# Kernel tuning notes

Hardware: AMD Instinct MI355X
Metric: run time of the kernel (lower is better)

Reference implementation:

```python
import jax, jax.numpy as jnp
import numpy as np

N, M, FEAT, POS, D, MSG, NCLS = 64, 32, 256, 6, 262, 128, 7


def setup_inputs() -> dict:
    key = jax.random.key(0)
    ks = jax.random.split(key, 12)
    s = 0.05
    p = lambda k, shape: jax.random.normal(k, shape, jnp.float32) * s
    return {
        "nodes_feature": jax.random.normal(ks[0], (N, M, FEAT), jnp.float32),
        "pos": jax.random.normal(ks[1], (N, M, POS), jnp.float32),
        "num_rec": jax.random.randint(ks[2], (N,), 1, M + 1),
        "link_w1": p(ks[3], (D, 2 * D)),
        "link_b1": jnp.zeros((D,), jnp.float32),
        "link_w2": p(ks[4], (D,)),
        "link_b2": jnp.zeros((), jnp.float32),
        "msg_w": p(ks[5], (MSG, D)),
        "msg_b": jnp.zeros((MSG,), jnp.float32),
        "gru_w_ih": p(ks[6], (3 * D, MSG)),
        "gru_w_hh": p(ks[7], (3 * D, D)),
        "gru_b_ih": jnp.zeros((3 * D,), jnp.float32),
        "gru_b_hh": jnp.zeros((3 * D,), jnp.float32),
        "ro_w1": p(ks[8], (MSG, D)),
        "ro_b1": jnp.zeros((MSG,), jnp.float32),
        "ro_w2": p(ks[9], (NCLS, MSG)),
        "ro_b2": jnp.zeros((NCLS,), jnp.float32),
    }


def reference(nodes_feature, pos, num_rec, link_w1, link_b1, link_w2, link_b2,
              msg_w, msg_b, gru_w_ih, gru_w_hh, gru_b_ih, gru_b_hh,
              ro_w1, ro_b1, ro_w2, ro_b2):
    # node_feat = [resnet_feat, pos]  -> (N, M, 262)
    nf = jnp.concatenate([nodes_feature, pos], axis=-1)
    n, m, d = nf.shape
    valid = jnp.arange(m)[None, :] < num_rec[:, None]          # (N, M)
    pair = valid[:, :, None] & valid[:, None, :]               # (N, M, M)

    # edge_feat[b,:,i,j] = concat(nf[b,i], nf[b,j]); zero for invalid pairs
    ef = jnp.concatenate([
        jnp.broadcast_to(nf[:, :, None, :], (n, m, m, d)),
        jnp.broadcast_to(nf[:, None, :, :], (n, m, m, d)),
    ], axis=-1) * pair[..., None].astype(nf.dtype)             # (N, M, M, 2D)

    # 1x1 convs == per-pair MLP
    hlink = jax.nn.relu(jnp.einsum('bnwc,dc->bnwd', ef, link_w1) + link_b1)
    attmat = jax.nn.sigmoid(jnp.einsum('bnwd,d->bnw', hlink, link_w2) + link_b2)

    # messages are only summed over valid sender nodes w
    att_m = attmat * valid[:, None, :].astype(attmat.dtype)    # (N, M, M)

    def gru_step(x, h):
        # PyTorch GRU cell: gates order (r, z, n)
        gx = x @ gru_w_ih.T + gru_b_ih
        gh = h @ gru_w_hh.T + gru_b_hh
        xr, xz, xn = jnp.split(gx, 3, axis=-1)
        hr, hz, hn = jnp.split(gh, 3, axis=-1)
        r = jax.nn.sigmoid(xr + hr)
        z = jax.nn.sigmoid(xz + hz)
        c = jnp.tanh(xn + r * hn)
        return (1.0 - z) * c + z * h

    vmask = valid[..., None].astype(nf.dtype)
    h_state = nf                                               # pass 0 input state
    for _ in range(2):                                         # two message-passing rounds
        msg = h_state @ msg_w.T + msg_b                        # (N, M, 128)
        m_v = jnp.einsum('bnw,bwk->bnk', att_m, msg)           # attention-weighted sum
        h_state = gru_step(m_v, h_state) * vmask               # invalid nodes stay zero

    pred = (jax.nn.relu(h_state @ ro_w1.T + ro_b1) @ ro_w2.T + ro_b2) * vmask
    return pred, attmat
```

## Files before the change

kernel.cpp:

```cpp
#include <hip/hip_runtime.h>
#include <math.h>

#define N_G   64
#define M_N   32
#define FEAT  256
#define POSD  6
#define D     262
#define MSG   128
#define NCLS  7

#define KA_S  424
#define PSTR  320

#define O_WPROJ 0u
#define O_WMSG  76032u
#define O_WRZ   94464u
#define O_WXN   207616u
#define O_WHN   225024u
#define O_WRO   264192u
#define O_WRO2  282624u
#define O_GB    283648u

typedef __attribute__((ext_vector_type(8))) short short8;
typedef __attribute__((ext_vector_type(4))) short short4v;
typedef __attribute__((ext_vector_type(4))) float floatx4;

#define MFMA __builtin_amdgcn_mfma_f32_16x16x32_bf16

__device__ __forceinline__ short f2bf(float f) {
    union { float f; unsigned u; } v; v.f = f;
    unsigned r = v.u + 0x7FFF + ((v.u >> 16) & 1);
    return (short)(r >> 16);
}
__device__ __forceinline__ float bf2f(short s) {
    union { float f; unsigned u; } v;
    v.u = ((unsigned)(unsigned short)s) << 16;
    return v.f;
}
__device__ __forceinline__ float sigf(float x) {
    return __builtin_amdgcn_rcpf(1.f + __expf(-x));
}
__device__ __forceinline__ float tanh_fast(float x) {
    float e = __expf(-2.f * fabsf(x));
    float t = (1.f - e) * __builtin_amdgcn_rcpf(1.f + e);
    return copysignf(t, x);
}

__global__ __launch_bounds__(256) void prep_kernel(
    const float* __restrict__ w1, const float* __restrict__ msg_w,
    const float* __restrict__ w_ih, const float* __restrict__ w_hh,
    const float* __restrict__ ro_w1, const float* __restrict__ ro_w2,
    const float* __restrict__ b_ih, const float* __restrict__ b_hh,
    float* __restrict__ ws)
{
    short* wproj = (short*)(ws + O_WPROJ);
    short* wmsg  = (short*)(ws + O_WMSG);
    short* wrz   = (short*)(ws + O_WRZ);
    short* wxn   = (short*)(ws + O_WXN);
    short* whn   = (short*)(ws + O_WHN);
    short* wro   = (short*)(ws + O_WRO);
    short* wro2  = (short*)(ws + O_WRO2);
    float* gb    = ws + O_GB;

    int job = blockIdx.x * 4 + (threadIdx.x >> 6);
    const int lane = threadIdx.x & 63;
    if (job >= 1112) return;
    const int lrow = lane & 15, quad = lane >> 4;

    if (job < 297) {
        const int s = job / 9, kk = job % 9;
        const int n = s * 16 + lrow, kb = quad * 8 + kk * 32;
        short8 o;
#pragma unroll
        for (int e = 0; e < 8; ++e) {
            int k = kb + e;
            float v = 0.f;
            if (k < D && n < 524)
                v = (n < D) ? w1[n * 524 + k] : w1[(n - D) * 524 + D + k];
            o[e] = f2bf(v);
        }
        *(short8*)(wproj + job * 512 + lane * 8) = o;
        return;
    }
    job -= 297;
    if (job < 72) {
        const int s = job / 9, kk = job % 9;
        const int n = s * 16 + lrow, kb = quad * 8 + kk * 32;
        short8 o;
#pragma unroll
        for (int e = 0; e < 8; ++e) {
            int k = kb + e;
            o[e] = f2bf(k < D ? msg_w[n * D + k] : 0.f);
        }
        *(short8*)(wmsg + job * 512 + lane * 8) = o;
        return;
    }
    job -= 72;
    if (job < 442) {
        const int gi = job >= 221;
        const int jj = job - gi * 221;
        const int s = jj / 13, kk = jj % 13;
        const int d = s * 16 + lrow, kb = quad * 8 + kk * 32;
        short8 o;
#pragma unroll
        for (int e = 0; e < 8; ++e) {
            int k = kb + e;
            float v = 0.f;
            if (d < D) {
                int r = gi * D + d;
                if (k < 128)          v = w_ih[r * MSG + k];
                else if (k < 128 + D) v = w_hh[r * D + (k - 128)];
            }
            o[e] = f2bf(v);
        }
        *(short8*)(wrz + job * 512 + lane * 8) = o;
        return;
    }
    job -= 442;
    if (job < 68) {
        const int s = job / 4, kk = job % 4;
        const int d = s * 16 + lrow, kb = quad * 8 + kk * 32;
        short8 o;
#pragma unroll
        for (int e = 0; e < 8; ++e) {
            int k = kb + e;
            o[e] = f2bf(d < D ? w_ih[(2 * D + d) * MSG + k] : 0.f);
        }
        *(short8*)(wxn + job * 512 + lane * 8) = o;
        return;
    }
    job -= 68;
    if (job < 153) {
        const int s = job / 9, kk = job % 9;
        const int d = s * 16 + lrow, kb = quad * 8 + kk * 32;
        short8 o;
#pragma unroll
        for (int e = 0; e < 8; ++e) {
            int k = kb + e;
            o[e] = f2bf((d < D && k < D) ? w_hh[(2 * D + d) * D + k] : 0.f);
        }
        *(short8*)(whn + job * 512 + lane * 8) = o;
        return;
    }
    job -= 153;
    if (job < 72) {
        const int s = job / 9, kk = job % 9;
        const int n = s * 16 + lrow, kb = quad * 8 + kk * 32;
        short8 o;
#pragma unroll
        for (int e = 0; e < 8; ++e) {
            int k = kb + e;
            o[e] = f2bf(k < D ? ro_w1[n * D + k] : 0.f);
        }
        *(short8*)(wro + job * 512 + lane * 8) = o;
        return;
    }
    job -= 72;
    if (job < 4) {
        const int kk = job;
        const int n = lrow, kb = quad * 8 + kk * 32;
        short8 o;
#pragma unroll
        for (int e = 0; e < 8; ++e) {
            int k = kb + e;
            o[e] = f2bf(n < NCLS ? ro_w2[n * MSG + k] : 0.f);
        }
        *(short8*)(wro2 + job * 512 + lane * 8) = o;
        return;
    }
    job -= 4;
    {
        const int seg = job;
        float* out = gb + seg * 272;
        for (int d = lane; d < 272; d += 64) {
            float v = 0.f;
            if (d < D) {
                if (seg == 0)      v = b_ih[d] + b_hh[d];
                else if (seg == 1) v = b_ih[D + d] + b_hh[D + d];
                else if (seg == 2) v = b_ih[2 * D + d];
                else               v = b_hh[2 * D + d];
            }
            out[d] = v;
        }
    }
}

__global__ __launch_bounds__(512, 2) void fused_kernel(
    const float* __restrict__ nodes, const float* __restrict__ pos,
    const int* __restrict__ nrec_g,
    const float* __restrict__ b1g, const float* __restrict__ w2g,
    const float* __restrict__ b2g, const float* __restrict__ msg_bg,
    const float* __restrict__ ro_b1g, const float* __restrict__ ro_b2g,
    const float* __restrict__ ws,
    float* __restrict__ att_out, float* __restrict__ pred)
{
    const short* Wproj = (const short*)(ws + O_WPROJ);
    const short* Wmsg  = (const short*)(ws + O_WMSG);
    const short* Wrz   = (const short*)(ws + O_WRZ);
    const short* Wxn   = (const short*)(ws + O_WXN);
    const short* Whn   = (const short*)(ws + O_WHN);
    const short* Wro   = (const short*)(ws + O_WRO);
    const short* Wro2  = (const short*)(ws + O_WRO2);
    const float* gb    = ws + O_GB;

    __shared__ __align__(16) short bufA[32 * KA_S];
    __shared__ __align__(16) short bufB[32 * KA_S];
    __shared__ __align__(16) short paL[32 * PSTR];
    __shared__ __align__(16) short pbL[32 * PSTR];
    __shared__ __align__(16) short attL[32 * 40];
    __shared__ __align__(16) short msgT[128 * 40];
    __shared__ __align__(16) short hidL[32 * 136];
    __shared__ __align__(16) float b1L[PSTR], w2L[PSTR];

    const int b = blockIdx.x;
    const int tid = threadIdx.x;
    const int wave = tid >> 6, lane = tid & 63;
    const int quad = lane >> 4, lrow = lane & 15;

    floatx4 prm[10];
    {
        const floatx4* pb = (const floatx4*)(ws + O_WRZ);
        const int base = wave * 64 + lane;
#pragma unroll
        for (int p = 0; p < 10; ++p)
            prm[p] = pb[(p * 512 + base) * 8];
    }
    short8 wvA[9];
    {
        const short* bw = Wproj + wave * 9 * 512 + lane * 8;
#pragma unroll
        for (int kk = 0; kk < 9; ++kk) wvA[kk] = *(const short8*)(bw + kk * 512);
    }

    const int nr = nrec_g[b];

    for (int idx = tid; idx < 32 * 64; idx += 512) {
        int w = idx >> 6, c4 = idx & 63;
        floatx4 v = *(const floatx4*)(nodes + ((size_t)(b * 32 + w)) * FEAT + c4 * 4);
        short4v s; s[0] = f2bf(v[0]); s[1] = f2bf(v[1]); s[2] = f2bf(v[2]); s[3] = f2bf(v[3]);
        *(short4v*)(bufA + w * KA_S + 128 + c4 * 4) = s;
    }
    for (int idx = tid; idx < 32 * POSD; idx += 512) {
        int w = idx / POSD, c = idx % POSD;
        bufA[w * KA_S + 128 + FEAT + c] = f2bf(pos[((size_t)(b * 32 + w)) * POSD + c]);
    }
    for (int idx = tid; idx < 32 * 34; idx += 512) {
        int w = idx / 34, c = idx % 34;
        bufA[w * KA_S + 390 + c] = 0;
        bufB[w * KA_S + 390 + c] = 0;
    }
    for (int idx = tid; idx < 32 * (PSTR - D); idx += 512) {
        int w = idx / (PSTR - D), c = idx % (PSTR - D);
        paL[w * PSTR + D + c] = 0;
        pbL[w * PSTR + D + c] = 0;
    }
    for (int d = tid; d < PSTR; d += 512) {
        b1L[d] = (d < D) ? b1g[d] : 0.f;
        w2L[d] = (d < D) ? w2g[d] : 0.f;
    }
#pragma unroll
    for (int p = 0; p < 10; ++p) asm volatile("" :: "v"(prm[p]));
    __syncthreads();

    {
        auto store_proj = [&](int s, floatx4 acc0, floatx4 acc1) {
            int col = s * 16 + lrow;
#pragma unroll
            for (int rr = 0; rr < 4; ++rr) {
                int r0 = quad * 4 + rr;
                if (col < D) {
                    paL[r0 * PSTR + col] = f2bf(acc0[rr]);
                    paL[(r0 + 16) * PSTR + col] = f2bf(acc1[rr]);
                } else if (col < 2 * D) {
                    pbL[r0 * PSTR + (col - D)] = f2bf(acc0[rr]);
                    pbL[(r0 + 16) * PSTR + (col - D)] = f2bf(acc1[rr]);
                }
            }
        };
        auto store_msg = [&](int s, floatx4 acc0, floatx4 acc1) {
            int col = (s - 33) * 16 + lrow;
            float bias = msg_bg[col];
#pragma unroll
            for (int rr = 0; rr < 4; ++rr) {
                msgT[col * 40 + quad * 4 + rr] = f2bf(acc0[rr] + bias);
                msgT[col * 40 + 16 + quad * 4 + rr] = f2bf(acc1[rr] + bias);
            }
        };

        short8 aF0[9], aF1[9];
        {
            const short* ap = bufA + lrow * KA_S + 128 + quad * 8;
#pragma unroll
            for (int kk = 0; kk < 9; ++kk) {
                aF0[kk] = *(const short8*)(ap + kk * 32);
                aF1[kk] = *(const short8*)(ap + 16 * KA_S + kk * 32);
            }
#pragma unroll
            for (int kk = 0; kk < 9; ++kk)
                asm volatile("" : "+v"(aF0[kk]), "+v"(aF1[kk]));
        }
        short8 wvB[9];

#define P1_LOAD(DST, TT) do { \
            const short* bw_ = ((TT) < 33) \
                ? Wproj + (TT) * 9 * 512 + lane * 8 \
                : Wmsg + ((TT) - 33) * 9 * 512 + lane * 8; \
            _Pragma("unroll") \
            for (int kk = 0; kk < 9; ++kk) DST[kk] = *(const short8*)(bw_ + kk * 512); \
        } while (0)

#define P1_TILE(W, TT) do { \
            floatx4 acc0_ = {}, acc1_ = {}; \
            _Pragma("unroll") \
            for (int kk = 0; kk < 9; ++kk) { \
                acc0_ = MFMA(aF0[kk], W[kk], acc0_, 0, 0, 0); \
                acc1_ = MFMA(aF1[kk], W[kk], acc1_, 0, 0, 0); \
            } \
            if ((TT) < 33) store_proj((TT), acc0_, acc1_); \
            else store_msg((TT), acc0_, acc1_); \
        } while (0)

        int t = wave;
        P1_LOAD(wvB, t + 8);
        P1_TILE(wvA, t);
        t += 8;
        P1_LOAD(wvA, t + 8);
        P1_TILE(wvB, t);
        t += 8;
        P1_LOAD(wvB, t + 8);
        P1_TILE(wvA, t);
        t += 8;
        P1_LOAD(wvA, t + 8);
        P1_TILE(wvB, t);
        t += 8;
        if (t + 8 < 41) P1_LOAD(wvB, t + 8);
        P1_TILE(wvA, t);
        t += 8;
        if (t < 41) P1_TILE(wvB, t);
#undef P1_LOAD
#undef P1_TILE
    }
    __syncthreads();

    {
        const int grp = tid >> 4;
        const int c16 = tid & 15;
        const float b2v = b2g[0];
        float pav[5][4], b1v[5][4], w2v[5][4];
#pragma unroll
        for (int k = 0; k < 5; ++k) {
            int dbase = c16 * 4 + 64 * k;
            short4v p = *(const short4v*)(paL + grp * PSTR + dbase);
            floatx4 bb = *(const floatx4*)(b1L + dbase);
            floatx4 ww = *(const floatx4*)(w2L + dbase);
#pragma unroll
            for (int e = 0; e < 4; ++e) {
                pav[k][e] = bf2f(p[e]); b1v[k][e] = bb[e]; w2v[k][e] = ww[e];
            }
        }
        float p0 = 0.f;
#pragma unroll
        for (int k = 0; k < 5; ++k)
#pragma unroll
            for (int e = 0; e < 4; ++e)
                p0 += fmaxf(b1v[k][e], 0.f) * w2v[k][e];
        p0 += __shfl_down(p0, 8, 16); p0 += __shfl_down(p0, 4, 16);
        p0 += __shfl_down(p0, 2, 16); p0 += __shfl_down(p0, 1, 16);
        float c0 = sigf(p0 + b2v);
        const bool vi = grp < nr;
        for (int j = 0; j < 32; ++j) {
            float a;
            if (j < nr && vi) {
                const short* pb = pbL + j * PSTR + c16 * 4;
                float s = 0.f;
#pragma unroll
                for (int k = 0; k < 5; ++k) {
                    short4v q = *(const short4v*)(pb + 64 * k);
#pragma unroll
                    for (int e = 0; e < 4; ++e) {
                        float v = pav[k][e] + bf2f(q[e]) + b1v[k][e];
                        s += fmaxf(v, 0.f) * w2v[k][e];
                    }
                }
                s += __shfl_down(s, 8, 16); s += __shfl_down(s, 4, 16);
                s += __shfl_down(s, 2, 16); s += __shfl_down(s, 1, 16);
                a = sigf(s + b2v);
            } else {
                a = c0;
            }
            if (c16 == 0) {
                att_out[((size_t)(b * 32 + grp)) * 32 + j] = a;
                attL[grp * 40 + j] = f2bf((j < nr) ? a : 0.f);
            }
        }
    }
    __syncthreads();

    for (int rnd = 0; rnd < 2; ++rnd) {
        short* src = rnd ? bufB : bufA;
        short* dst = rnd ? bufA : bufB;

        if (rnd) {
            int s = wave;
            const short* bw = Wmsg + s * 9 * 512 + lane * 8;
            short8 wm[9];
#pragma unroll
            for (int kk = 0; kk < 9; ++kk) wm[kk] = *(const short8*)(bw + kk * 512);
            floatx4 acc0 = {}, acc1 = {};
            const short* ap = src + lrow * KA_S + 128 + quad * 8;
#pragma unroll
            for (int kk = 0; kk < 9; ++kk) {
                short8 x0 = *(const short8*)(ap + kk * 32);
                short8 x1 = *(const short8*)(ap + 16 * KA_S + kk * 32);
                acc0 = MFMA(x0, wm[kk], acc0, 0, 0, 0);
                acc1 = MFMA(x1, wm[kk], acc1, 0, 0, 0);
            }
            int col = s * 16 + lrow;
            float bias = msg_bg[col];
#pragma unroll
            for (int rr = 0; rr < 4; ++rr) {
                msgT[col * 40 + quad * 4 + rr] = f2bf(acc0[rr] + bias);
                msgT[col * 40 + 16 + quad * 4 + rr] = f2bf(acc1[rr] + bias);
            }
            __syncthreads();
        }

        {
            int mi = wave & 1, ng = wave >> 1;
            short8 afrag = *(const short8*)(attL + (mi * 16 + lrow) * 40 + quad * 8);
            floatx4 acc0 = {}, acc1 = {};
            short8 bf0 = *(const short8*)(msgT + (ng * 32 + lrow) * 40 + quad * 8);
            short8 bf1 = *(const short8*)(msgT + (ng * 32 + 16 + lrow) * 40 + quad * 8);
            acc0 = MFMA(afrag, bf0, acc0, 0, 0, 0);
            acc1 = MFMA(afrag, bf1, acc1, 0, 0, 0);
#pragma unroll
            for (int rr = 0; rr < 4; ++rr) {
                int m = mi * 16 + quad * 4 + rr;
                src[m * KA_S + ng * 32 + lrow] = f2bf(acc0[rr]);
                src[m * KA_S + ng * 32 + 16 + lrow] = f2bf(acc1[rr]);
            }
        }
        __syncthreads();

        {
            short8 aA0[13], aA1[13];
            {
                const short* ap0 = src + lrow * KA_S + quad * 8;
#pragma unroll
                for (int kk = 0; kk < 13; ++kk) {
                    aA0[kk] = *(const short8*)(ap0 + kk * 32);
                    aA1[kk] = *(const short8*)(ap0 + 16 * KA_S + kk * 32);
                }
#pragma unroll
                for (int kk = 0; kk < 13; ++kk)
                    asm volatile("" : "+v"(aA0[kk]), "+v"(aA1[kk]));
            }
            for (int s = wave; s < 17; s += 8) {
                const short* bpr = Wrz + (s * 13) * 512 + lane * 8;
                const short* bpz = Wrz + (221 + s * 13) * 512 + lane * 8;
                const short* bpx = Wxn + (s * 4) * 512 + lane * 8;
                const short* bph = Whn + (s * 9) * 512 + lane * 8;

                short8 wr[13];
#pragma unroll
                for (int kk = 0; kk < 13; ++kk) wr[kk] = *(const short8*)(bpr + kk * 512);
#pragma unroll
                for (int kk = 0; kk < 13; ++kk) asm volatile("" : "+v"(wr[kk]));

                floatx4 aR0 = {}, aR1 = {}, aZ0 = {}, aZ1 = {};
                floatx4 aN0 = {}, aN1 = {}, aH0 = {}, aH1 = {};
#pragma unroll
                for (int kk = 0; kk < 13; ++kk) {
                    aR0 = MFMA(aA0[kk], wr[kk], aR0, 0, 0, 0);
                    aR1 = MFMA(aA1[kk], wr[kk], aR1, 0, 0, 0);
                    if (kk < 4) {
                        short8 bx = *(const short8*)(bpx + kk * 512);
                        aN0 = MFMA(aA0[kk], bx, aN0, 0, 0, 0);
                        aN1 = MFMA(aA1[kk], bx, aN1, 0, 0, 0);
                    }
                    wr[kk] = *(const short8*)(bpz + kk * 512);
                }
#pragma unroll
                for (int kk = 0; kk < 13; ++kk) {
                    aZ0 = MFMA(aA0[kk], wr[kk], aZ0, 0, 0, 0);
                    aZ1 = MFMA(aA1[kk], wr[kk], aZ1, 0, 0, 0);
                    if (kk < 9) wr[kk] = *(const short8*)(bph + kk * 512);
                }
#pragma unroll
                for (int kk = 0; kk < 9; ++kk) {
                    aH0 = MFMA(aA0[kk + 4], wr[kk], aH0, 0, 0, 0);
                    aH1 = MFMA(aA1[kk + 4], wr[kk], aH1, 0, 0, 0);
                }

                int d = s * 16 + lrow;
                if (d < D) {
                    float bgr = gb[d], bgz = gb[272 + d];
                    float bxv = gb[544 + d], bhv = gb[816 + d];
#pragma unroll
                    for (int i = 0; i < 2; ++i) {
                        floatx4 vR = i ? aR1 : aR0, vZ = i ? aZ1 : aZ0;
                        floatx4 vN = i ? aN1 : aN0, vH = i ? aH1 : aH0;
#pragma unroll
                        for (int rr = 0; rr < 4; ++rr) {
                            int m = i * 16 + quad * 4 + rr;
                            float rg = sigf(vR[rr] + bgr);
                            float zg = sigf(vZ[rr] + bgz);
                            float cg = tanh_fast(vN[rr] + bxv + rg * (vH[rr] + bhv));
                            float hold = bf2f(src[m * KA_S + 128 + d]);
                            float hv = (1.f - zg) * cg + zg * hold;
                            if (m >= nr) hv = 0.f;
                            dst[m * KA_S + 128 + d] = f2bf(hv);
                        }
                    }
                }
            }
        }
        __syncthreads();
    }

    {
        int s = wave;
        const short* bw = Wro + s * 9 * 512 + lane * 8;
        short8 wv[9];
#pragma unroll
        for (int kk = 0; kk < 9; ++kk) wv[kk] = *(const short8*)(bw + kk * 512);
        floatx4 acc0 = {}, acc1 = {};
        const short* ap = bufA + lrow * KA_S + 128 + quad * 8;
#pragma unroll
        for (int kk = 0; kk < 9; ++kk) {
            short8 x0 = *(const short8*)(ap + kk * 32);
            short8 x1 = *(const short8*)(ap + 16 * KA_S + kk * 32);
            acc0 = MFMA(x0, wv[kk], acc0, 0, 0, 0);
            acc1 = MFMA(x1, wv[kk], acc1, 0, 0, 0);
        }
        int col = s * 16 + lrow;
        float bias = ro_b1g[col];
#pragma unroll
        for (int rr = 0; rr < 4; ++rr) {
            hidL[(quad * 4 + rr) * 136 + col] = f2bf(fmaxf(acc0[rr] + bias, 0.f));
            hidL[(16 + quad * 4 + rr) * 136 + col] = f2bf(fmaxf(acc1[rr] + bias, 0.f));
        }
    }
    __syncthreads();

    if (wave == 0) {
        const short* bw = Wro2 + lane * 8;
        short8 wv[4];
#pragma unroll
        for (int kk = 0; kk < 4; ++kk) wv[kk] = *(const short8*)(bw + kk * 512);
        floatx4 acc0 = {}, acc1 = {};
        const short* ap = hidL + lrow * 136 + quad * 8;
#pragma unroll
        for (int kk = 0; kk < 4; ++kk) {
            short8 x0 = *(const short8*)(ap + kk * 32);
            short8 x1 = *(const short8*)(ap + 16 * 136 + kk * 32);
            acc0 = MFMA(x0, wv[kk], acc0, 0, 0, 0);
            acc1 = MFMA(x1, wv[kk], acc1, 0, 0, 0);
        }
        int q = lrow;
        if (q < NCLS) {
            float bias = ro_b2g[q];
#pragma unroll
            for (int i = 0; i < 2; ++i) {
#pragma unroll
                for (int rr = 0; rr < 4; ++rr) {
                    int m = i * 16 + quad * 4 + rr;
                    float v = (i ? acc1[rr] : acc0[rr]) + bias;
                    if (m >= nr) v = 0.f;
                    pred[((size_t)(b * 32 + m)) * NCLS + q] = v;
                }
            }
        }
    }
}

extern "C" void kernel_launch(void* const* d_in, const int* in_sizes, int n_in,
                              void* d_out, int out_size, void* d_ws, size_t ws_size,
                              hipStream_t stream)
{
    const float* nodes = (const float*)d_in[0];
    const float* pos   = (const float*)d_in[1];
    const int*   nrec  = (const int*)d_in[2];
    const float* w1    = (const float*)d_in[3];
    const float* b1    = (const float*)d_in[4];
    const float* w2    = (const float*)d_in[5];
    const float* b2    = (const float*)d_in[6];
    const float* msg_w = (const float*)d_in[7];
    const float* msg_b = (const float*)d_in[8];
    const float* w_ih  = (const float*)d_in[9];
    const float* w_hh  = (const float*)d_in[10];
    const float* b_ih  = (const float*)d_in[11];
    const float* b_hh  = (const float*)d_in[12];
    const float* ro_w1 = (const float*)d_in[13];
    const float* ro_b1 = (const float*)d_in[14];
    const float* ro_w2 = (const float*)d_in[15];
    const float* ro_b2 = (const float*)d_in[16];
    float* ws   = (float*)d_ws;
    float* pred = (float*)d_out;
    float* attout = pred + (size_t)N_G * M_N * NCLS;

    prep_kernel<<<278, 256, 0, stream>>>(w1, msg_w, w_ih, w_hh, ro_w1, ro_w2,
                                         b_ih, b_hh, ws);
    fused_kernel<<<N_G, 512, 0, stream>>>(nodes, pos, nrec, b1, w2, b2, msg_b,
                                          ro_b1, ro_b2, ws, attout, pred);
}
```

Before: 137.4 us.

## Double block size to 1024 threads and redistribute work across sixteen waves

Each block now launches 1024 threads instead of 512, and every phase is re-split across 16 waves. The projection tiles, attention rows (each thread group handles half the columns), message and readout MFMAs (one 16-row half per wave) and the GRU gate tiles are all divided more finely. Register-held A fragments and prefetched weights are dropped in favour of per-iteration LDS and global loads, which frees registers for the larger block. The aim is more latency hiding on a grid of only 64 blocks, at the cost of more LDS and global load traffic and a poorly balanced GRU loop with 17 tiles spread over 16 waves.

```diff
diff --git a/kernel.cpp b/kernel.cpp
--- a/kernel.cpp
+++ b/kernel.cpp
@@ -185,7 +185,7 @@
     }
 }
 
-__global__ __launch_bounds__(512, 2) void fused_kernel(
+__global__ __launch_bounds__(1024, 4) void fused_kernel(
     const float* __restrict__ nodes, const float* __restrict__ pos,
     const int* __restrict__ nrec_g,
     const float* __restrict__ b1g, const float* __restrict__ w2g,
@@ -216,14 +216,15 @@
     const int tid = threadIdx.x;
     const int wave = tid >> 6, lane = tid & 63;
     const int quad = lane >> 4, lrow = lane & 15;
-
-    floatx4 prm[10];
+    const int nr = nrec_g[b];
+
+    floatx4 prm[6];
     {
         const floatx4* pb = (const floatx4*)(ws + O_WRZ);
         const int base = wave * 64 + lane;
 #pragma unroll
-        for (int p = 0; p < 10; ++p)
-            prm[p] = pb[(p * 512 + base) * 8];
+        for (int p = 0; p < 6; ++p)
+            prm[p] = pb[(p * 1024 + base) * 8];
     }
     short8 wvA[9];
     {
@@ -232,34 +233,32 @@
         for (int kk = 0; kk < 9; ++kk) wvA[kk] = *(const short8*)(bw + kk * 512);
     }
 
-    const int nr = nrec_g[b];
-
-    for (int idx = tid; idx < 32 * 64; idx += 512) {
+    for (int idx = tid; idx < 32 * 64; idx += 1024) {
         int w = idx >> 6, c4 = idx & 63;
         floatx4 v = *(const floatx4*)(nodes + ((size_t)(b * 32 + w)) * FEAT + c4 * 4);
         short4v s; s[0] = f2bf(v[0]); s[1] = f2bf(v[1]); s[2] = f2bf(v[2]); s[3] = f2bf(v[3]);
         *(short4v*)(bufA + w * KA_S + 128 + c4 * 4) = s;
     }
-    for (int idx = tid; idx < 32 * POSD; idx += 512) {
+    for (int idx = tid; idx < 32 * POSD; idx += 1024) {
         int w = idx / POSD, c = idx % POSD;
         bufA[w * KA_S + 128 + FEAT + c] = f2bf(pos[((size_t)(b * 32 + w)) * POSD + c]);
     }
-    for (int idx = tid; idx < 32 * 34; idx += 512) {
+    for (int idx = tid; idx < 32 * 34; idx += 1024) {
         int w = idx / 34, c = idx % 34;
         bufA[w * KA_S + 390 + c] = 0;
         bufB[w * KA_S + 390 + c] = 0;
     }
-    for (int idx = tid; idx < 32 * (PSTR - D); idx += 512) {
+    for (int idx = tid; idx < 32 * (PSTR - D); idx += 1024) {
         int w = idx / (PSTR - D), c = idx % (PSTR - D);
         paL[w * PSTR + D + c] = 0;
         pbL[w * PSTR + D + c] = 0;
     }
-    for (int d = tid; d < PSTR; d += 512) {
+    for (int d = tid; d < PSTR; d += 1024) {
         b1L[d] = (d < D) ? b1g[d] : 0.f;
         w2L[d] = (d < D) ? w2g[d] : 0.f;
     }
 #pragma unroll
-    for (int p = 0; p < 10; ++p) asm volatile("" :: "v"(prm[p]));
+    for (int p = 0; p < 6; ++p) asm volatile("" :: "v"(prm[p]));
     __syncthreads();
 
     {
@@ -286,19 +285,7 @@
                 msgT[col * 40 + 16 + quad * 4 + rr] = f2bf(acc1[rr] + bias);
             }
         };
-
-        short8 aF0[9], aF1[9];
-        {
-            const short* ap = bufA + lrow * KA_S + 128 + quad * 8;
-#pragma unroll
-            for (int kk = 0; kk < 9; ++kk) {
-                aF0[kk] = *(const short8*)(ap + kk * 32);
-                aF1[kk] = *(const short8*)(ap + 16 * KA_S + kk * 32);
-            }
-#pragma unroll
-            for (int kk = 0; kk < 9; ++kk)
-                asm volatile("" : "+v"(aF0[kk]), "+v"(aF1[kk]));
-        }
+        const short* ap = bufA + lrow * KA_S + 128 + quad * 8;
         short8 wvB[9];
 
 #define P1_LOAD(DST, TT) do { \
@@ -313,30 +300,22 @@
             floatx4 acc0_ = {}, acc1_ = {}; \
             _Pragma("unroll") \
             for (int kk = 0; kk < 9; ++kk) { \
-                acc0_ = MFMA(aF0[kk], W[kk], acc0_, 0, 0, 0); \
-                acc1_ = MFMA(aF1[kk], W[kk], acc1_, 0, 0, 0); \
+                short8 x0 = *(const short8*)(ap + kk * 32); \
+                short8 x1 = *(const short8*)(ap + 16 * KA_S + kk * 32); \
+                acc0_ = MFMA(x0, W[kk], acc0_, 0, 0, 0); \
+                acc1_ = MFMA(x1, W[kk], acc1_, 0, 0, 0); \
             } \
             if ((TT) < 33) store_proj((TT), acc0_, acc1_); \
             else store_msg((TT), acc0_, acc1_); \
         } while (0)
 
-        int t = wave;
-        P1_LOAD(wvB, t + 8);
-        P1_TILE(wvA, t);
-        t += 8;
-        P1_LOAD(wvA, t + 8);
-        P1_TILE(wvB, t);
-        t += 8;
-        P1_LOAD(wvB, t + 8);
-        P1_TILE(wvA, t);
-        t += 8;
-        P1_LOAD(wvA, t + 8);
-        P1_TILE(wvB, t);
-        t += 8;
-        if (t + 8 < 41) P1_LOAD(wvB, t + 8);
-        P1_TILE(wvA, t);
-        t += 8;
-        if (t < 41) P1_TILE(wvB, t);
+        const int t0 = wave, t1 = wave + 16, t2 = wave + 32;
+        P1_LOAD(wvB, t1);
+        P1_TILE(wvA, t0);
+        const bool has2 = t2 < 41;
+        if (has2) P1_LOAD(wvA, t2);
+        P1_TILE(wvB, t1);
+        if (has2) P1_TILE(wvA, t2);
 #undef P1_LOAD
 #undef P1_TILE
     }
@@ -344,13 +323,15 @@
 
     {
         const int grp = tid >> 4;
+        const int i   = grp >> 1;
+        const int jh  = (grp & 1) * 16;
         const int c16 = tid & 15;
         const float b2v = b2g[0];
         float pav[5][4], b1v[5][4], w2v[5][4];
 #pragma unroll
         for (int k = 0; k < 5; ++k) {
             int dbase = c16 * 4 + 64 * k;
-            short4v p = *(const short4v*)(paL + grp * PSTR + dbase);
+            short4v p = *(const short4v*)(paL + i * PSTR + dbase);
             floatx4 bb = *(const floatx4*)(b1L + dbase);
             floatx4 ww = *(const floatx4*)(w2L + dbase);
 #pragma unroll
@@ -367,8 +348,9 @@
         p0 += __shfl_down(p0, 8, 16); p0 += __shfl_down(p0, 4, 16);
         p0 += __shfl_down(p0, 2, 16); p0 += __shfl_down(p0, 1, 16);
         float c0 = sigf(p0 + b2v);
-        const bool vi = grp < nr;
-        for (int j = 0; j < 32; ++j) {
+        const bool vi = i < nr;
+        for (int jj = 0; jj < 16; ++jj) {
+            int j = jh + jj;
             float a;
             if (j < nr && vi) {
                 const short* pb = pbL + j * PSTR + c16 * 4;
@@ -389,8 +371,8 @@
                 a = c0;
             }
             if (c16 == 0) {
-                att_out[((size_t)(b * 32 + grp)) * 32 + j] = a;
-                attL[grp * 40 + j] = f2bf((j < nr) ? a : 0.f);
+                att_out[((size_t)(b * 32 + i)) * 32 + j] = a;
+                attL[i * 40 + j] = f2bf((j < nr) ? a : 0.f);
             }
         }
     }
@@ -401,116 +383,89 @@
         short* dst = rnd ? bufA : bufB;
 
         if (rnd) {
-            int s = wave;
+            int s = wave >> 1, mi = wave & 1;
             const short* bw = Wmsg + s * 9 * 512 + lane * 8;
             short8 wm[9];
 #pragma unroll
             for (int kk = 0; kk < 9; ++kk) wm[kk] = *(const short8*)(bw + kk * 512);
-            floatx4 acc0 = {}, acc1 = {};
-            const short* ap = src + lrow * KA_S + 128 + quad * 8;
+            floatx4 acc = {};
+            const short* ap = src + (mi * 16 + lrow) * KA_S + 128 + quad * 8;
 #pragma unroll
             for (int kk = 0; kk < 9; ++kk) {
-                short8 x0 = *(const short8*)(ap + kk * 32);
-                short8 x1 = *(const short8*)(ap + 16 * KA_S + kk * 32);
-                acc0 = MFMA(x0, wm[kk], acc0, 0, 0, 0);
-                acc1 = MFMA(x1, wm[kk], acc1, 0, 0, 0);
+                short8 a0 = *(const short8*)(ap + kk * 32);
+                acc = MFMA(a0, wm[kk], acc, 0, 0, 0);
             }
             int col = s * 16 + lrow;
             float bias = msg_bg[col];
 #pragma unroll
-            for (int rr = 0; rr < 4; ++rr) {
-                msgT[col * 40 + quad * 4 + rr] = f2bf(acc0[rr] + bias);
-                msgT[col * 40 + 16 + quad * 4 + rr] = f2bf(acc1[rr] + bias);
-            }
+            for (int rr = 0; rr < 4; ++rr)
+                msgT[col * 40 + mi * 16 + quad * 4 + rr] = f2bf(acc[rr] + bias);
             __syncthreads();
         }
 
         {
             int mi = wave & 1, ng = wave >> 1;
             short8 afrag = *(const short8*)(attL + (mi * 16 + lrow) * 40 + quad * 8);
-            floatx4 acc0 = {}, acc1 = {};
-            short8 bf0 = *(const short8*)(msgT + (ng * 32 + lrow) * 40 + quad * 8);
-            short8 bf1 = *(const short8*)(msgT + (ng * 32 + 16 + lrow) * 40 + quad * 8);
-            acc0 = MFMA(afrag, bf0, acc0, 0, 0, 0);
-            acc1 = MFMA(afrag, bf1, acc1, 0, 0, 0);
+            floatx4 acc = {};
+            short8 bf0 = *(const short8*)(msgT + (ng * 16 + lrow) * 40 + quad * 8);
+            acc = MFMA(afrag, bf0, acc, 0, 0, 0);
 #pragma unroll
             for (int rr = 0; rr < 4; ++rr) {
                 int m = mi * 16 + quad * 4 + rr;
-                src[m * KA_S + ng * 32 + lrow] = f2bf(acc0[rr]);
-                src[m * KA_S + ng * 32 + 16 + lrow] = f2bf(acc1[rr]);
+                src[m * KA_S + ng * 16 + lrow] = f2bf(acc[rr]);
             }
         }
         __syncthreads();
 
-        {
-            short8 aA0[13], aA1[13];
-            {
-                const short* ap0 = src + lrow * KA_S + quad * 8;
-#pragma unroll
-                for (int kk = 0; kk < 13; ++kk) {
-                    aA0[kk] = *(const short8*)(ap0 + kk * 32);
-                    aA1[kk] = *(const short8*)(ap0 + 16 * KA_S + kk * 32);
+        for (int s = wave; s < 17; s += 16) {
+            const short* ap0 = src + lrow * KA_S + quad * 8;
+            const short* ap1 = ap0 + 16 * KA_S;
+            const short* bpr = Wrz + (s * 13) * 512 + lane * 8;
+            const short* bpz = Wrz + (221 + s * 13) * 512 + lane * 8;
+            const short* bpx = Wxn + (s * 4) * 512 + lane * 8;
+            const short* bph = Whn + (s * 9) * 512 + lane * 8;
+
+            floatx4 aR0 = {}, aR1 = {}, aZ0 = {}, aZ1 = {};
+            floatx4 aN0 = {}, aN1 = {}, aH0 = {}, aH1 = {};
+#pragma unroll
+            for (int kk = 0; kk < 13; ++kk) {
+                short8 x0 = *(const short8*)(ap0 + kk * 32);
+                short8 x1 = *(const short8*)(ap1 + kk * 32);
+                short8 br = *(const short8*)(bpr + kk * 512);
+                short8 bz = *(const short8*)(bpz + kk * 512);
+                aR0 = MFMA(x0, br, aR0, 0, 0, 0);
+                aR1 = MFMA(x1, br, aR1, 0, 0, 0);
+                aZ0 = MFMA(x0, bz, aZ0, 0, 0, 0);
+                aZ1 = MFMA(x1, bz, aZ1, 0, 0, 0);
+                if (kk < 4) {
+                    short8 bx = *(const short8*)(bpx + kk * 512);
+                    aN0 = MFMA(x0, bx, aN0, 0, 0, 0);
+                    aN1 = MFMA(x1, bx, aN1, 0, 0, 0);
+                } else {
+                    short8 bh = *(const short8*)(bph + (kk - 4) * 512);
+                    aH0 = MFMA(x0, bh, aH0, 0, 0, 0);
+                    aH1 = MFMA(x1, bh, aH1, 0, 0, 0);
                 }
-#pragma unroll
-                for (int kk = 0; kk < 13; ++kk)
-                    asm volatile("" : "+v"(aA0[kk]), "+v"(aA1[kk]));
-            }
-            for (int s = wave; s < 17; s += 8) {
-                const short* bpr = Wrz + (s * 13) * 512 + lane * 8;
-                const short* bpz = Wrz + (221 + s * 13) * 512 + lane * 8;
-                const short* bpx = Wxn + (s * 4) * 512 + lane * 8;
-                const short* bph = Whn + (s * 9) * 512 + lane * 8;
-
-                short8 wr[13];
-#pragma unroll
-                for (int kk = 0; kk < 13; ++kk) wr[kk] = *(const short8*)(bpr + kk * 512);
-#pragma unroll
-                for (int kk = 0; kk < 13; ++kk) asm volatile("" : "+v"(wr[kk]));
-
-                floatx4 aR0 = {}, aR1 = {}, aZ0 = {}, aZ1 = {};
-                floatx4 aN0 = {}, aN1 = {}, aH0 = {}, aH1 = {};
-#pragma unroll
-                for (int kk = 0; kk < 13; ++kk) {
-                    aR0 = MFMA(aA0[kk], wr[kk], aR0, 0, 0, 0);
-                    aR1 = MFMA(aA1[kk], wr[kk], aR1, 0, 0, 0);
-                    if (kk < 4) {
-                        short8 bx = *(const short8*)(bpx + kk * 512);
-                        aN0 = MFMA(aA0[kk], bx, aN0, 0, 0, 0);
-                        aN1 = MFMA(aA1[kk], bx, aN1, 0, 0, 0);
-                    }
-                    wr[kk] = *(const short8*)(bpz + kk * 512);
-                }
-#pragma unroll
-                for (int kk = 0; kk < 13; ++kk) {
-                    aZ0 = MFMA(aA0[kk], wr[kk], aZ0, 0, 0, 0);
-                    aZ1 = MFMA(aA1[kk], wr[kk], aZ1, 0, 0, 0);
-                    if (kk < 9) wr[kk] = *(const short8*)(bph + kk * 512);
-                }
-#pragma unroll
-                for (int kk = 0; kk < 9; ++kk) {
-                    aH0 = MFMA(aA0[kk + 4], wr[kk], aH0, 0, 0, 0);
-                    aH1 = MFMA(aA1[kk + 4], wr[kk], aH1, 0, 0, 0);
-                }
-
-                int d = s * 16 + lrow;
-                if (d < D) {
-                    float bgr = gb[d], bgz = gb[272 + d];
-                    float bxv = gb[544 + d], bhv = gb[816 + d];
-#pragma unroll
-                    for (int i = 0; i < 2; ++i) {
-                        floatx4 vR = i ? aR1 : aR0, vZ = i ? aZ1 : aZ0;
-                        floatx4 vN = i ? aN1 : aN0, vH = i ? aH1 : aH0;
-#pragma unroll
-                        for (int rr = 0; rr < 4; ++rr) {
-                            int m = i * 16 + quad * 4 + rr;
-                            float rg = sigf(vR[rr] + bgr);
-                            float zg = sigf(vZ[rr] + bgz);
-                            float cg = tanh_fast(vN[rr] + bxv + rg * (vH[rr] + bhv));
-                            float hold = bf2f(src[m * KA_S + 128 + d]);
-                            float hv = (1.f - zg) * cg + zg * hold;
-                            if (m >= nr) hv = 0.f;
-                            dst[m * KA_S + 128 + d] = f2bf(hv);
-                        }
+            }
+
+            int d = s * 16 + lrow;
+            if (d < D) {
+                float bgr = gb[d], bgz = gb[272 + d];
+                float bxv = gb[544 + d], bhv = gb[816 + d];
+#pragma unroll
+                for (int i = 0; i < 2; ++i) {
+                    floatx4 vR = i ? aR1 : aR0, vZ = i ? aZ1 : aZ0;
+                    floatx4 vN = i ? aN1 : aN0, vH = i ? aH1 : aH0;
+#pragma unroll
+                    for (int rr = 0; rr < 4; ++rr) {
+                        int m = i * 16 + quad * 4 + rr;
+                        float rg = sigf(vR[rr] + bgr);
+                        float zg = sigf(vZ[rr] + bgz);
+                        float cg = tanh_fast(vN[rr] + bxv + rg * (vH[rr] + bhv));
+                        float hold = bf2f(src[m * KA_S + 128 + d]);
+                        float hv = (1.f - zg) * cg + zg * hold;
+                        if (m >= nr) hv = 0.f;
+                        dst[m * KA_S + 128 + d] = f2bf(hv);
                     }
                 }
             }
@@ -519,56 +474,47 @@
     }
 
     {
-        int s = wave;
+        int s = wave >> 1, mi = wave & 1;
         const short* bw = Wro + s * 9 * 512 + lane * 8;
         short8 wv[9];
 #pragma unroll
         for (int kk = 0; kk < 9; ++kk) wv[kk] = *(const short8*)(bw + kk * 512);
-        floatx4 acc0 = {}, acc1 = {};
-        const short* ap = bufA + lrow * KA_S + 128 + quad * 8;
+        floatx4 acc = {};
+        const short* ap = bufA + (mi * 16 + lrow) * KA_S + 128 + quad * 8;
 #pragma unroll
         for (int kk = 0; kk < 9; ++kk) {
-            short8 x0 = *(const short8*)(ap + kk * 32);
-            short8 x1 = *(const short8*)(ap + 16 * KA_S + kk * 32);
-            acc0 = MFMA(x0, wv[kk], acc0, 0, 0, 0);
-            acc1 = MFMA(x1, wv[kk], acc1, 0, 0, 0);
+            short8 a0 = *(const short8*)(ap + kk * 32);
+            acc = MFMA(a0, wv[kk], acc, 0, 0, 0);
         }
         int col = s * 16 + lrow;
         float bias = ro_b1g[col];
 #pragma unroll
-        for (int rr = 0; rr < 4; ++rr) {
-            hidL[(quad * 4 + rr) * 136 + col] = f2bf(fmaxf(acc0[rr] + bias, 0.f));
-            hidL[(16 + quad * 4 + rr) * 136 + col] = f2bf(fmaxf(acc1[rr] + bias, 0.f));
-        }
+        for (int rr = 0; rr < 4; ++rr)
+            hidL[(mi * 16 + quad * 4 + rr) * 136 + col] = f2bf(fmaxf(acc[rr] + bias, 0.f));
     }
     __syncthreads();
 
-    if (wave == 0) {
+    if (wave < 2) {
         const short* bw = Wro2 + lane * 8;
         short8 wv[4];
 #pragma unroll
         for (int kk = 0; kk < 4; ++kk) wv[kk] = *(const short8*)(bw + kk * 512);
-        floatx4 acc0 = {}, acc1 = {};
-        const short* ap = hidL + lrow * 136 + quad * 8;
+        floatx4 acc = {};
+        const short* ap = hidL + (wave * 16 + lrow) * 136 + quad * 8;
 #pragma unroll
         for (int kk = 0; kk < 4; ++kk) {
-            short8 x0 = *(const short8*)(ap + kk * 32);
-            short8 x1 = *(const short8*)(ap + 16 * 136 + kk * 32);
-            acc0 = MFMA(x0, wv[kk], acc0, 0, 0, 0);
-            acc1 = MFMA(x1, wv[kk], acc1, 0, 0, 0);
+            short8 a0 = *(const short8*)(ap + kk * 32);
+            acc = MFMA(a0, wv[kk], acc, 0, 0, 0);
         }
         int q = lrow;
         if (q < NCLS) {
             float bias = ro_b2g[q];
 #pragma unroll
-            for (int i = 0; i < 2; ++i) {
-#pragma unroll
-                for (int rr = 0; rr < 4; ++rr) {
-                    int m = i * 16 + quad * 4 + rr;
-                    float v = (i ? acc1[rr] : acc0[rr]) + bias;
-                    if (m >= nr) v = 0.f;
-                    pred[((size_t)(b * 32 + m)) * NCLS + q] = v;
-                }
+            for (int rr = 0; rr < 4; ++rr) {
+                int m = wave * 16 + quad * 4 + rr;
+                float v = acc[rr] + bias;
+                if (m >= nr) v = 0.f;
+                pred[((size_t)(b * 32 + m)) * NCLS + q] = v;
             }
         }
     }
@@ -601,6 +547,6 @@
 
     prep_kernel<<<278, 256, 0, stream>>>(w1, msg_w, w_ih, w_hh, ro_w1, ro_w2,
                                          b_ih, b_hh, ws);
-    fused_kernel<<<N_G, 512, 0, stream>>>(nodes, pos, nrec, b1, w2, b2, msg_b,
-                                          ro_b1, ro_b2, ws, attout, pred);
-}
+    fused_kernel<<<N_G, 1024, 0, stream>>>(nodes, pos, nrec, b1, w2, b2, msg_b,
+                                           ro_b1, ro_b2, ws, attout, pred);
+}
```

Result: slower. 168.4 us (+22.5%).
